# Kernel tuning notes

Measured on AMD Instinct MI355X. Metric: run time of the kernel, lower is better.

Reference implementation:

```python
import jax, jax.numpy as jnp
import numpy as np

ALPHA = 0.2          # LeakyReLU slope
NEG_BIG = -9e15      # mask value from the torch code
LN_EPS = 1e-5        # torch LayerNorm default eps
GAT_SCALE = 1.0


def _layer_norm(x, g, b):
    mu = x.mean(-1, keepdims=True)
    var = ((x - mu) ** 2).mean(-1, keepdims=True)
    return (x - mu) * jax.lax.rsqrt(var + LN_EPS) * g + b


def _gat_layer(h, adj, W, a, concat):
    # h: [B,N,Fin], adj: [N,N] weighted, W: [Fin,Fout], a: [2*Fout,1]
    Wh = jnp.einsum('bnf,fo->bno', h, W)                 # [B,N,Fout]
    Fo = W.shape[1]
    a_i, a_j = a[:Fo, 0], a[Fo:, 0]
    # e[b,i,j] = leakyrelu(Wh[b,i].a_i + Wh[b,j].a_j)  (== cat([Wh_i,Wh_j]) @ a)
    e = jax.nn.leaky_relu(
        (Wh @ a_i)[:, :, None] + (Wh @ a_j)[:, None, :], ALPHA)  # [B,N,N]
    att = jnp.where(adj[None, :, :] > 0, e, NEG_BIG)
    att = jax.nn.softmax(att, axis=2)
    att = att * adj[None, :, :]
    att = att / (att.sum(axis=2, keepdims=True) + 1e-8)
    h_prime = jnp.einsum('bij,bjo->bio', att, Wh)        # [B,N,Fout]
    return jax.nn.elu(h_prime) if concat else h_prime


def setup_inputs() -> dict:
    B, N, H, ID = 1024, 128, 64, 8
    GIN = 1 + ID  # node_feat_dim = 0
    key = jax.random.key(0)
    ks = jax.random.split(key, 20)
    # sparse weighted adjacency with self-loops
    w = jax.random.uniform(ks[0], (N, N))
    m = (jax.random.uniform(ks[1], (N, N)) < 0.3).astype(jnp.float32)
    adj = w * m + jnp.eye(N, dtype=jnp.float32)
    sc = lambda k, s: jax.random.normal(k, s, jnp.float32) * 0.1
    return {
        'c_values': jax.random.normal(ks[2], (B, N), jnp.float32),
        'adj': adj,
        'agent_emb': sc(ks[3], (N, ID)),
        'W1': sc(ks[4], (GIN, H)), 'a1': sc(ks[5], (2 * H, 1)),
        'W2': sc(ks[6], (H, H)),   'a2': sc(ks[7], (2 * H, 1)),
        'ln1_g': jnp.ones((H,)), 'ln1_b': jnp.zeros((H,)),
        'ln2_g': jnp.ones((H,)), 'ln2_b': jnp.zeros((H,)),
        'head_gat_w': sc(ks[8], (H, 1)), 'head_gat_b': jnp.zeros((1,)),
        'mlp1_w': sc(ks[9], (N, H)),  'mlp1_b': jnp.zeros((H,)),
        'mlp2_w': sc(ks[10], (H, H)), 'mlp2_b': jnp.zeros((H,)),
        'head_mlp_w': sc(ks[11], (H, 1)), 'head_mlp_b': jnp.zeros((1,)),
        'gate1_w': sc(ks[12], (N, H)), 'gate1_b': jnp.zeros((H,)),
        'gate2_w': sc(ks[13], (H, 1)), 'gate2_b': jnp.full((1,), -5.0),
    }


def reference(c_values, adj, agent_emb, W1, a1, W2, a2,
              ln1_g, ln1_b, ln2_g, ln2_b, head_gat_w, head_gat_b,
              mlp1_w, mlp1_b, mlp2_w, mlp2_b, head_mlp_w, head_mlp_b,
              gate1_w, gate1_b, gate2_w, gate2_b):
    B, N = c_values.shape
    # node features: [c_value, agent_id_embedding]
    id_feat = jnp.broadcast_to(agent_emb[None], (B, N, agent_emb.shape[1]))
    x_g = jnp.concatenate([c_values[..., None], id_feat], axis=-1)  # [B,N,9]
    h1 = _gat_layer(x_g, adj, W1, a1, concat=True)
    h1 = _layer_norm(h1, ln1_g, ln1_b)
    h2 = _gat_layer(h1, adj, W2, a2, concat=False)
    h = jax.nn.relu(h2 + h1)
    h = _layer_norm(h, ln2_g, ln2_b)
    q_gat = h.mean(axis=1) @ head_gat_w + head_gat_b                # [B,1]
    x_m = jax.nn.relu(c_values @ mlp1_w + mlp1_b)
    x_m = jax.nn.relu(x_m @ mlp2_w + mlp2_b)
    q_mlp = x_m @ head_mlp_w + head_mlp_b                           # [B,1]
    gate = jax.nn.sigmoid(
        jax.nn.relu(c_values @ gate1_w + gate1_b) @ gate2_w + gate2_b)
    return q_mlp + gate * GAT_SCALE * q_gat
```

## Files before the change

### kernel.cpp

```cpp
#include <hip/hip_runtime.h>

typedef unsigned short u16;
typedef unsigned int u32;
typedef short v8s __attribute__((ext_vector_type(8)));
typedef float v4f __attribute__((ext_vector_type(4)));

__device__ __forceinline__ float bflo(u32 d){union{u32 i;float f;}u;u.i=d<<16;return u.f;}
__device__ __forceinline__ float bfhi(u32 d){union{u32 i;float f;}u;u.i=d&0xffff0000u;return u.f;}
__device__ __forceinline__ u16 f2bfr(float f){union{float f;u32 i;}u;u.f=f;return (u16)((u.i+0x8000u)>>16);}
__device__ __forceinline__ u32 pk2bf(float a,float b){
    union{float f;u32 i;}ua,ub; ua.f=a; ub.f=b;
    return ((ua.i+0x8000u)>>16)|((ub.i+0x8000u)&0xffff0000u);
}
__device__ __forceinline__ v8s pack8(const float* w){
    union { uint4 u; v8s v; } c;
    c.u.x = pk2bf(w[0],w[1]); c.u.y = pk2bf(w[2],w[3]);
    c.u.z = pk2bf(w[4],w[5]); c.u.w = pk2bf(w[6],w[7]);
    return c.v;
}

__device__ __forceinline__ void flash_att(
    int wv, int l15, int q4,
    const float* __restrict__ ADJ,
    const float* __restrict__ sEi, const float* __restrict__ sFi,
    const float* __restrict__ sEj, const float* __restrict__ sFj,
    const u16* __restrict__ sWhT,
    v4f acc[2][4], float invD[2])
{
    const int r0 = 16*wv + l15, r1 = r0 + 64;
    const float Ei0 = sEi[r0], Fi0 = sFi[r0];
    const float Ei1 = sEi[r1], Fi1 = sFi[r1];
    float D0 = 0.f, D1 = 0.f;
    #pragma unroll
    for (int s = 0; s < 2; ++s)
        #pragma unroll
        for (int ct = 0; ct < 4; ++ct) acc[s][ct] = (v4f){0.f,0.f,0.f,0.f};

    for (int ks = 0; ks < 4; ++ks) {
        const int ko = ks*32 + q4*8;
        float w0[8], w1[8];
        #pragma unroll
        for (int half = 0; half < 2; ++half) {
            float4 E4 = *(const float4*)(sEj + ko + 4*half);
            float4 F4 = *(const float4*)(sFj + ko + 4*half);
            float4 a0 = *(const float4*)(ADJ + r0*128 + ko + 4*half);
            float4 a1 = *(const float4*)(ADJ + r1*128 + ko + 4*half);
            float Ev[4] = {E4.x,E4.y,E4.z,E4.w};
            float Fv[4] = {F4.x,F4.y,F4.z,F4.w};
            float av0[4] = {a0.x,a0.y,a0.z,a0.w};
            float av1[4] = {a1.x,a1.y,a1.z,a1.w};
            #pragma unroll
            for (int k = 0; k < 4; ++k) {
                float p0 = Ei0 * Ev[k], q0 = Fi0 * Fv[k];
                float s0 = (p0 >= 1.f) ? p0 : q0;
                float x0 = s0 * av0[k];
                float p1 = Ei1 * Ev[k], q1 = Fi1 * Fv[k];
                float s1 = (p1 >= 1.f) ? p1 : q1;
                float x1 = s1 * av1[k];
                w0[half*4 + k] = x0; w1[half*4 + k] = x1;
                D0 += x0; D1 += x1;
            }
        }
        v8s A0 = pack8(w0), A1 = pack8(w1);
        #pragma unroll
        for (int ct = 0; ct < 4; ++ct) {
            v8s B = *(const v8s*)(sWhT + (16*ct + l15)*136 + ko);
            acc[0][ct] = __builtin_amdgcn_mfma_f32_16x16x32_bf16(A0, B, acc[0][ct], 0,0,0);
            acc[1][ct] = __builtin_amdgcn_mfma_f32_16x16x32_bf16(A1, B, acc[1][ct], 0,0,0);
        }
    }
    D0 += __shfl_xor(D0, 16); D0 += __shfl_xor(D0, 32);
    D1 += __shfl_xor(D1, 16); D1 += __shfl_xor(D1, 32);
    invD[0] = 1.f / D0; invD[1] = 1.f / D1;
}

__global__ __launch_bounds__(256, 4) void graphmixer_kernel(
    const float* __restrict__ C,
    const float* __restrict__ ADJ,
    const float* __restrict__ EMB,
    const float* __restrict__ W1,
    const float* __restrict__ A1,
    const float* __restrict__ W2,
    const float* __restrict__ A2,
    const float* __restrict__ LN1G, const float* __restrict__ LN1B,
    const float* __restrict__ LN2G, const float* __restrict__ LN2B,
    const float* __restrict__ HGW,  const float* __restrict__ HGB,
    const float* __restrict__ MLP1W, const float* __restrict__ MLP1B,
    const float* __restrict__ MLP2W, const float* __restrict__ MLP2B,
    const float* __restrict__ HMW,  const float* __restrict__ HMB,
    const float* __restrict__ G1W,  const float* __restrict__ G1B,
    const float* __restrict__ G2W,  const float* __restrict__ G2B,
    float* __restrict__ OUT)
{
    const int b = blockIdx.x, t = threadIdx.x;
    const int lane = t & 63, wv = t >> 6;
    const int l15 = lane & 15, q4 = lane >> 4;

    __shared__ __align__(16) unsigned char smem[40096];
    u16*   sWhT = (u16*)(smem);
    u16*   sH1  = (u16*)(smem + 17408);
    float* sEi  = (float*)(smem + 35840);
    float* sFi  = (float*)(smem + 36352);
    float* sEj  = (float*)(smem + 36864);
    float* sFj  = (float*)(smem + 37376);
    float* colp = (float*)(smem + 37888);
    float* sScr = (float*)(smem + 38912);
    float* v2i  = (float*)(smem + 39456);
    float* v2j  = (float*)(smem + 39712);
    float* v1i  = (float*)(smem + 39968);
    float* v1j  = (float*)(smem + 40032);
    float* sEmb = (float*)(smem + 17408);
    float* sC   = (float*)(smem + 21504);

    const float* Cb = C + b*128;

    if (wv == 0) {
        #pragma unroll
        for (int q = 0; q < 4; ++q)
            ((float4*)sEmb)[lane + 64*q] = ((const float4*)EMB)[lane + 64*q];
        if (lane < 32) ((float4*)sC)[lane] = ((const float4*)Cb)[lane];
        if (lane >= 32 && lane < 41) {
            int f = lane - 32; float a = 0.f;
            for (int q = 0; q < 16; ++q) {
                float4 w = *(const float4*)(W1 + f*64 + q*4);
                float4 x = *(const float4*)(A1 + q*4);
                a += w.x*x.x + w.y*x.y + w.z*x.z + w.w*x.w;
            }
            v1i[f] = a;
        } else if (lane >= 48 && lane < 57) {
            int f = lane - 48; float a = 0.f;
            for (int q = 0; q < 16; ++q) {
                float4 w = *(const float4*)(W1 + f*64 + q*4);
                float4 x = *(const float4*)(A1 + 64 + q*4);
                a += w.x*x.x + w.y*x.y + w.z*x.z + w.w*x.w;
            }
            v1j[f] = a;
        }
    } else if (wv == 3) {
        float ai = 0.f, aj = 0.f;
        for (int q = 0; q < 16; ++q) {
            float4 w  = *(const float4*)(W2 + lane*64 + q*4);
            float4 xi = *(const float4*)(A2 + q*4);
            float4 xj = *(const float4*)(A2 + 64 + q*4);
            ai += w.x*xi.x + w.y*xi.y + w.z*xi.z + w.w*xi.w;
            aj += w.x*xj.x + w.y*xj.y + w.z*xj.z + w.w*xj.w;
        }
        v2i[lane] = ai; v2j[lane] = aj;
    } else if (wv == 1) {
        float a = 0.f;
        for (int k = 0; k < 128; k += 4) {
            float4 c4 = *(const float4*)(Cb + k);
            a += c4.x*MLP1W[k*64+lane] + c4.y*MLP1W[(k+1)*64+lane]
               + c4.z*MLP1W[(k+2)*64+lane] + c4.w*MLP1W[(k+3)*64+lane];
        }
        sScr[lane] = fmaxf(a + MLP1B[lane], 0.f);
        float a2 = 0.f;
        for (int k = 0; k < 64; ++k) a2 += sScr[k] * MLP2W[k*64 + lane];
        float x2 = fmaxf(a2 + MLP2B[lane], 0.f);
        float p1 = x2 * HMW[lane];
        #pragma unroll
        for (int off = 32; off >= 1; off >>= 1) p1 += __shfl_down(p1, off);
        if (lane == 0) sScr[128] = p1 + HMB[0];
    } else {
        float a = 0.f;
        for (int k = 0; k < 128; k += 4) {
            float4 c4 = *(const float4*)(Cb + k);
            a += c4.x*G1W[k*64+lane] + c4.y*G1W[(k+1)*64+lane]
               + c4.z*G1W[(k+2)*64+lane] + c4.w*G1W[(k+3)*64+lane];
        }
        float g1 = fmaxf(a + G1B[lane], 0.f);
        float p2 = g1 * G2W[lane];
        #pragma unroll
        for (int off = 32; off >= 1; off >>= 1) p2 += __shfl_down(p2, off);
        if (lane == 0) sScr[129] = 1.f / (1.f + __expf(-(p2 + G2B[0])));
    }
    __syncthreads();

    {
        const int o = lane, cc = wv;
        float w1f[9];
        #pragma unroll
        for (int f = 0; f < 9; ++f) w1f[f] = W1[f*64 + o];
        float whv[32];
        for (int i = 0; i < 32; ++i) {
            const int ig = cc*32 + i;
            float a = sC[ig] * w1f[0];
            float4 e0 = *(const float4*)(sEmb + ig*8);
            float4 e1 = *(const float4*)(sEmb + ig*8 + 4);
            a += e0.x*w1f[1] + e0.y*w1f[2] + e0.z*w1f[3] + e0.w*w1f[4];
            a += e1.x*w1f[5] + e1.y*w1f[6] + e1.z*w1f[7] + e1.w*w1f[8];
            whv[i] = a;
        }
        u32 p[16];
        #pragma unroll
        for (int q = 0; q < 16; ++q) p[q] = pk2bf(whv[2*q], whv[2*q+1]);
        uint4* dst = (uint4*)(sWhT + o*136 + cc*32);
        dst[0] = ((uint4*)p)[0]; dst[1] = ((uint4*)p)[1];
        dst[2] = ((uint4*)p)[2]; dst[3] = ((uint4*)p)[3];
    }
    if (t < 128) {
        float c = sC[t];
        float4 e0 = *(const float4*)(sEmb + t*8);
        float4 e1 = *(const float4*)(sEmb + t*8 + 4);
        float ei = c*v1i[0] + e0.x*v1i[1]+e0.y*v1i[2]+e0.z*v1i[3]+e0.w*v1i[4]
                            + e1.x*v1i[5]+e1.y*v1i[6]+e1.z*v1i[7]+e1.w*v1i[8];
        float ej = c*v1j[0] + e0.x*v1j[1]+e0.y*v1j[2]+e0.z*v1j[3]+e0.w*v1j[4]
                            + e1.x*v1j[5]+e1.y*v1j[6]+e1.z*v1j[7]+e1.w*v1j[8];
        sEi[t] = __expf(ei); sFi[t] = __expf(0.2f*ei);
        sEj[t] = __expf(ej); sFj[t] = __expf(0.2f*ej);
    }
    __syncthreads();

    {
        v4f acc[2][4]; float invD[2];
        flash_att(wv, l15, q4, ADJ, sEi, sFi, sEj, sFj, sWhT, acc, invD);

        float g4[4], b4[4];
        #pragma unroll
        for (int ct = 0; ct < 4; ++ct) { g4[ct] = LN1G[16*ct + l15]; b4[ct] = LN1B[16*ct + l15]; }
        #pragma unroll
        for (int s = 0; s < 2; ++s) {
            const int rbase = 16*(wv + 4*s) + 4*q4;
            #pragma unroll
            for (int reg = 0; reg < 4; ++reg) {
                const int row = rbase + reg;
                const float rd = __shfl(invD[s], 4*q4 + reg);
                float x[4], s1 = 0.f, s2 = 0.f;
                #pragma unroll
                for (int ct = 0; ct < 4; ++ct) {
                    float v = acc[s][ct][reg] * rd;
                    v = (v > 0.f) ? v : (__expf(v) - 1.f);
                    x[ct] = v; s1 += v; s2 += v*v;
                }
                s1 += __shfl_xor(s1, 1); s2 += __shfl_xor(s2, 1);
                s1 += __shfl_xor(s1, 2); s2 += __shfl_xor(s2, 2);
                s1 += __shfl_xor(s1, 4); s2 += __shfl_xor(s2, 4);
                s1 += __shfl_xor(s1, 8); s2 += __shfl_xor(s2, 8);
                const float mean = s1 * (1.f/64.f);
                const float var  = s2 * (1.f/64.f) - mean*mean;
                const float rstd = rsqrtf(var + 1e-5f);
                #pragma unroll
                for (int ct = 0; ct < 4; ++ct) {
                    float h = (x[ct] - mean) * rstd * g4[ct] + b4[ct];
                    sH1[row*72 + 16*ct + l15] = f2bfr(h);
                }
            }
        }
    }
    __syncthreads();

    if (t < 128) {
        float ei = 0.f, ej = 0.f;
        const u16* hrow = sH1 + t*72;
        for (int q = 0; q < 16; ++q) {
            uint2 d = *(const uint2*)(hrow + q*4);
            float h0 = bflo(d.x), h1v = bfhi(d.x), h2 = bflo(d.y), h3 = bfhi(d.y);
            ei += h0*v2i[q*4+0] + h1v*v2i[q*4+1] + h2*v2i[q*4+2] + h3*v2i[q*4+3];
            ej += h0*v2j[q*4+0] + h1v*v2j[q*4+1] + h2*v2j[q*4+2] + h3*v2j[q*4+3];
        }
        sEi[t] = __expf(ei); sFi[t] = __expf(0.2f*ei);
        sEj[t] = __expf(ej); sFj[t] = __expf(0.2f*ej);
    }
    {
        v4f acc2[2][4];
        #pragma unroll
        for (int s = 0; s < 2; ++s)
            #pragma unroll
            for (int ct = 0; ct < 4; ++ct) acc2[s][ct] = (v4f){0.f,0.f,0.f,0.f};
        #pragma unroll
        for (int ks = 0; ks < 2; ++ks) {
            const int kb = ks*32 + q4*8;
            v8s Bf[4];
            #pragma unroll
            for (int ct = 0; ct < 4; ++ct) {
                const float* wp = W2 + kb*64 + 16*ct + l15;
                float w8[8];
                #pragma unroll
                for (int j = 0; j < 8; ++j) w8[j] = wp[j*64];
                Bf[ct] = pack8(w8);
            }
            #pragma unroll
            for (int s = 0; s < 2; ++s) {
                v8s A = *(const v8s*)(sH1 + (16*(wv+4*s) + l15)*72 + kb);
                #pragma unroll
                for (int ct = 0; ct < 4; ++ct)
                    acc2[s][ct] = __builtin_amdgcn_mfma_f32_16x16x32_bf16(A, Bf[ct], acc2[s][ct], 0,0,0);
            }
        }
        #pragma unroll
        for (int s = 0; s < 2; ++s) {
            const int rb = 16*(wv+4*s) + 4*q4;
            #pragma unroll
            for (int ct = 0; ct < 4; ++ct) {
                const int col = 16*ct + l15;
                uint2 p;
                p.x = pk2bf(acc2[s][ct][0], acc2[s][ct][1]);
                p.y = pk2bf(acc2[s][ct][2], acc2[s][ct][3]);
                *(uint2*)(sWhT + col*136 + rb) = p;
            }
        }
    }
    __syncthreads();

    {
        v4f acc[2][4]; float invD[2];
        flash_att(wv, l15, q4, ADJ, sEi, sFi, sEj, sFj, sWhT, acc, invD);

        float g4[4], b4[4], colsum[4];
        #pragma unroll
        for (int ct = 0; ct < 4; ++ct) {
            g4[ct] = LN2G[16*ct + l15]; b4[ct] = LN2B[16*ct + l15]; colsum[ct] = 0.f;
        }
        #pragma unroll
        for (int s = 0; s < 2; ++s) {
            const int rbase = 16*(wv + 4*s) + 4*q4;
            #pragma unroll
            for (int reg = 0; reg < 4; ++reg) {
                const int row = rbase + reg;
                const float rd = __shfl(invD[s], 4*q4 + reg);
                float x[4], s1 = 0.f, s2 = 0.f;
                #pragma unroll
                for (int ct = 0; ct < 4; ++ct) {
                    float h1v = bflo((u32)sH1[row*72 + 16*ct + l15]);
                    float v = fmaxf(acc[s][ct][reg] * rd + h1v, 0.f);
                    x[ct] = v; s1 += v; s2 += v*v;
                }
                s1 += __shfl_xor(s1, 1); s2 += __shfl_xor(s2, 1);
                s1 += __shfl_xor(s1, 2); s2 += __shfl_xor(s2, 2);
                s1 += __shfl_xor(s1, 4); s2 += __shfl_xor(s2, 4);
                s1 += __shfl_xor(s1, 8); s2 += __shfl_xor(s2, 8);
                const float mean = s1 * (1.f/64.f);
                const float var  = s2 * (1.f/64.f) - mean*mean;
                const float rstd = rsqrtf(var + 1e-5f);
                #pragma unroll
                for (int ct = 0; ct < 4; ++ct)
                    colsum[ct] += (x[ct] - mean) * rstd * g4[ct] + b4[ct];
            }
        }
        #pragma unroll
        for (int ct = 0; ct < 4; ++ct) {
            colsum[ct] += __shfl_xor(colsum[ct], 16);
            colsum[ct] += __shfl_xor(colsum[ct], 32);
        }
        if (lane < 16) {
            #pragma unroll
            for (int ct = 0; ct < 4; ++ct) colp[wv*64 + ct*16 + lane] = colsum[ct];
        }
    }
    __syncthreads();

    if (wv == 0) {
        float s = colp[lane] + colp[64 + lane] + colp[128 + lane] + colp[192 + lane];
        float p = s * (1.f/128.f) * HGW[lane];
        #pragma unroll
        for (int off = 32; off >= 1; off >>= 1) p += __shfl_down(p, off);
        if (lane == 0) OUT[b] = sScr[128] + sScr[129] * (p + HGB[0]);
    }
}

extern "C" void kernel_launch(void* const* d_in, const int* in_sizes, int n_in,
                              void* d_out, int out_size, void* d_ws, size_t ws_size,
                              hipStream_t stream) {
    (void)n_in; (void)out_size; (void)d_ws; (void)ws_size;
    const float* C     = (const float*)d_in[0];
    const float* ADJ   = (const float*)d_in[1];
    const float* EMB   = (const float*)d_in[2];
    const float* W1    = (const float*)d_in[3];
    const float* A1    = (const float*)d_in[4];
    const float* W2    = (const float*)d_in[5];
    const float* A2    = (const float*)d_in[6];
    const float* LN1G  = (const float*)d_in[7];
    const float* LN1B  = (const float*)d_in[8];
    const float* LN2G  = (const float*)d_in[9];
    const float* LN2B  = (const float*)d_in[10];
    const float* HGW   = (const float*)d_in[11];
    const float* HGB   = (const float*)d_in[12];
    const float* MLP1W = (const float*)d_in[13];
    const float* MLP1B = (const float*)d_in[14];
    const float* MLP2W = (const float*)d_in[15];
    const float* MLP2B = (const float*)d_in[16];
    const float* HMW   = (const float*)d_in[17];
    const float* HMB   = (const float*)d_in[18];
    const float* G1W   = (const float*)d_in[19];
    const float* G1B   = (const float*)d_in[20];
    const float* G2W   = (const float*)d_in[21];
    const float* G2B   = (const float*)d_in[22];

    const int B = in_sizes[0] / 128;

    graphmixer_kernel<<<dim3(B), dim3(256), 0, stream>>>(
        C, ADJ, EMB, W1, A1, W2, A2, LN1G, LN1B, LN2G, LN2B,
        HGW, HGB, MLP1W, MLP1B, MLP2W, MLP2B, HMW, HMB,
        G1W, G1B, G2W, G2B, (float*)d_out);
}
```

Measured before the change: 131.4 us.

## Compute attention row sums via MFMA, use hardware bf16 packing, keep h1 in registers

Computes the attention denominators with an extra MFMA against a ones vector instead of scalar adds and cross-lane shuffles, which also places the sums in the same layout as the output accumulators. The LeakyReLU branch is replaced with an fmaxf, and the manual bf16 rounding is swapped for the HIP packed conversion intrinsic. The LayerNorm-1 output is kept packed in registers so the residual add in layer 2 does not re-read shared memory. Several small dot-product loops get multiple accumulators to break dependency chains. Risks include higher register pressure from the extra accumulators and h1 cache, plus slight numerical differences because the denominator is now summed from bf16-rounded weights.

```diff
diff --git a/kernel.cpp b/kernel.cpp
--- a/kernel.cpp
+++ b/kernel.cpp
@@ -1,4 +1,5 @@
 #include <hip/hip_runtime.h>
+#include <hip/hip_bf16.h>
 
 typedef unsigned short u16;
 typedef unsigned int u32;
@@ -7,15 +8,14 @@
 
 __device__ __forceinline__ float bflo(u32 d){union{u32 i;float f;}u;u.i=d<<16;return u.f;}
 __device__ __forceinline__ float bfhi(u32 d){union{u32 i;float f;}u;u.i=d&0xffff0000u;return u.f;}
-__device__ __forceinline__ u16 f2bfr(float f){union{float f;u32 i;}u;u.f=f;return (u16)((u.i+0x8000u)>>16);}
-__device__ __forceinline__ u32 pk2bf(float a,float b){
-    union{float f;u32 i;}ua,ub; ua.f=a; ub.f=b;
-    return ((ua.i+0x8000u)>>16)|((ub.i+0x8000u)&0xffff0000u);
+__device__ __forceinline__ u32 cvtpk(float a, float b){
+    __hip_bfloat162 h = __float22bfloat162_rn(make_float2(a, b));
+    u32 r; __builtin_memcpy(&r, &h, sizeof(r)); return r;
 }
 __device__ __forceinline__ v8s pack8(const float* w){
     union { uint4 u; v8s v; } c;
-    c.u.x = pk2bf(w[0],w[1]); c.u.y = pk2bf(w[2],w[3]);
-    c.u.z = pk2bf(w[4],w[5]); c.u.w = pk2bf(w[6],w[7]);
+    c.u.x = cvtpk(w[0],w[1]); c.u.y = cvtpk(w[2],w[3]);
+    c.u.z = cvtpk(w[4],w[5]); c.u.w = cvtpk(w[6],w[7]);
     return c.v;
 }
 
@@ -25,16 +25,18 @@
     const float* __restrict__ sEi, const float* __restrict__ sFi,
     const float* __restrict__ sEj, const float* __restrict__ sFj,
     const u16* __restrict__ sWhT,
-    v4f acc[2][4], float invD[2])
+    v4f acc[2][4], v4f accD[2])
 {
     const int r0 = 16*wv + l15, r1 = r0 + 64;
     const float Ei0 = sEi[r0], Fi0 = sFi[r0];
     const float Ei1 = sEi[r1], Fi1 = sFi[r1];
-    float D0 = 0.f, D1 = 0.f;
+    const v8s ONES = {16256,16256,16256,16256,16256,16256,16256,16256};
     #pragma unroll
-    for (int s = 0; s < 2; ++s)
+    for (int s = 0; s < 2; ++s) {
+        accD[s] = (v4f){0.f,0.f,0.f,0.f};
         #pragma unroll
         for (int ct = 0; ct < 4; ++ct) acc[s][ct] = (v4f){0.f,0.f,0.f,0.f};
+    }
 
     for (int ks = 0; ks < 4; ++ks) {
         const int ko = ks*32 + q4*8;
@@ -51,17 +53,13 @@
             float av1[4] = {a1.x,a1.y,a1.z,a1.w};
             #pragma unroll
             for (int k = 0; k < 4; ++k) {
-                float p0 = Ei0 * Ev[k], q0 = Fi0 * Fv[k];
-                float s0 = (p0 >= 1.f) ? p0 : q0;
-                float x0 = s0 * av0[k];
-                float p1 = Ei1 * Ev[k], q1 = Fi1 * Fv[k];
-                float s1 = (p1 >= 1.f) ? p1 : q1;
-                float x1 = s1 * av1[k];
-                w0[half*4 + k] = x0; w1[half*4 + k] = x1;
-                D0 += x0; D1 += x1;
+                w0[half*4 + k] = fmaxf(Ei0*Ev[k], Fi0*Fv[k]) * av0[k];
+                w1[half*4 + k] = fmaxf(Ei1*Ev[k], Fi1*Fv[k]) * av1[k];
             }
         }
         v8s A0 = pack8(w0), A1 = pack8(w1);
+        accD[0] = __builtin_amdgcn_mfma_f32_16x16x32_bf16(A0, ONES, accD[0], 0,0,0);
+        accD[1] = __builtin_amdgcn_mfma_f32_16x16x32_bf16(A1, ONES, accD[1], 0,0,0);
         #pragma unroll
         for (int ct = 0; ct < 4; ++ct) {
             v8s B = *(const v8s*)(sWhT + (16*ct + l15)*136 + ko);
@@ -69,9 +67,6 @@
             acc[1][ct] = __builtin_amdgcn_mfma_f32_16x16x32_bf16(A1, B, acc[1][ct], 0,0,0);
         }
     }
-    D0 += __shfl_xor(D0, 16); D0 += __shfl_xor(D0, 32);
-    D1 += __shfl_xor(D1, 16); D1 += __shfl_xor(D1, 32);
-    invD[0] = 1.f / D0; invD[1] = 1.f / D1;
 }
 
 __global__ __launch_bounds__(256, 4) void graphmixer_kernel(
@@ -120,55 +115,70 @@
             ((float4*)sEmb)[lane + 64*q] = ((const float4*)EMB)[lane + 64*q];
         if (lane < 32) ((float4*)sC)[lane] = ((const float4*)Cb)[lane];
         if (lane >= 32 && lane < 41) {
-            int f = lane - 32; float a = 0.f;
-            for (int q = 0; q < 16; ++q) {
+            int f = lane - 32; float a0 = 0.f, a1 = 0.f;
+            for (int q = 0; q < 16; q += 2) {
                 float4 w = *(const float4*)(W1 + f*64 + q*4);
                 float4 x = *(const float4*)(A1 + q*4);
-                a += w.x*x.x + w.y*x.y + w.z*x.z + w.w*x.w;
-            }
-            v1i[f] = a;
+                a0 += w.x*x.x + w.y*x.y + w.z*x.z + w.w*x.w;
+                float4 w2 = *(const float4*)(W1 + f*64 + (q+1)*4);
+                float4 x2 = *(const float4*)(A1 + (q+1)*4);
+                a1 += w2.x*x2.x + w2.y*x2.y + w2.z*x2.z + w2.w*x2.w;
+            }
+            v1i[f] = a0 + a1;
         } else if (lane >= 48 && lane < 57) {
-            int f = lane - 48; float a = 0.f;
-            for (int q = 0; q < 16; ++q) {
+            int f = lane - 48; float a0 = 0.f, a1 = 0.f;
+            for (int q = 0; q < 16; q += 2) {
                 float4 w = *(const float4*)(W1 + f*64 + q*4);
                 float4 x = *(const float4*)(A1 + 64 + q*4);
-                a += w.x*x.x + w.y*x.y + w.z*x.z + w.w*x.w;
-            }
-            v1j[f] = a;
+                a0 += w.x*x.x + w.y*x.y + w.z*x.z + w.w*x.w;
+                float4 w2 = *(const float4*)(W1 + f*64 + (q+1)*4);
+                float4 x2 = *(const float4*)(A1 + 64 + (q+1)*4);
+                a1 += w2.x*x2.x + w2.y*x2.y + w2.z*x2.z + w2.w*x2.w;
+            }
+            v1j[f] = a0 + a1;
         }
     } else if (wv == 3) {
-        float ai = 0.f, aj = 0.f;
+        float ai0 = 0.f, ai1 = 0.f, aj0 = 0.f, aj1 = 0.f;
         for (int q = 0; q < 16; ++q) {
             float4 w  = *(const float4*)(W2 + lane*64 + q*4);
             float4 xi = *(const float4*)(A2 + q*4);
             float4 xj = *(const float4*)(A2 + 64 + q*4);
-            ai += w.x*xi.x + w.y*xi.y + w.z*xi.z + w.w*xi.w;
-            aj += w.x*xj.x + w.y*xj.y + w.z*xj.z + w.w*xj.w;
-        }
-        v2i[lane] = ai; v2j[lane] = aj;
+            ai0 += w.x*xi.x + w.y*xi.y; ai1 += w.z*xi.z + w.w*xi.w;
+            aj0 += w.x*xj.x + w.y*xj.y; aj1 += w.z*xj.z + w.w*xj.w;
+        }
+        v2i[lane] = ai0 + ai1; v2j[lane] = aj0 + aj1;
     } else if (wv == 1) {
-        float a = 0.f;
+        float a0 = 0.f, a1 = 0.f, a2v = 0.f, a3 = 0.f;
         for (int k = 0; k < 128; k += 4) {
             float4 c4 = *(const float4*)(Cb + k);
-            a += c4.x*MLP1W[k*64+lane] + c4.y*MLP1W[(k+1)*64+lane]
-               + c4.z*MLP1W[(k+2)*64+lane] + c4.w*MLP1W[(k+3)*64+lane];
-        }
-        sScr[lane] = fmaxf(a + MLP1B[lane], 0.f);
-        float a2 = 0.f;
-        for (int k = 0; k < 64; ++k) a2 += sScr[k] * MLP2W[k*64 + lane];
-        float x2 = fmaxf(a2 + MLP2B[lane], 0.f);
+            a0  += c4.x*MLP1W[k*64+lane];
+            a1  += c4.y*MLP1W[(k+1)*64+lane];
+            a2v += c4.z*MLP1W[(k+2)*64+lane];
+            a3  += c4.w*MLP1W[(k+3)*64+lane];
+        }
+        sScr[lane] = fmaxf(a0+a1+a2v+a3 + MLP1B[lane], 0.f);
+        float b0 = 0.f, b1 = 0.f, b2 = 0.f, b3 = 0.f;
+        for (int k = 0; k < 64; k += 4) {
+            b0 += sScr[k]  *MLP2W[k*64 + lane];
+            b1 += sScr[k+1]*MLP2W[(k+1)*64 + lane];
+            b2 += sScr[k+2]*MLP2W[(k+2)*64 + lane];
+            b3 += sScr[k+3]*MLP2W[(k+3)*64 + lane];
+        }
+        float x2 = fmaxf(b0+b1+b2+b3 + MLP2B[lane], 0.f);
         float p1 = x2 * HMW[lane];
         #pragma unroll
         for (int off = 32; off >= 1; off >>= 1) p1 += __shfl_down(p1, off);
         if (lane == 0) sScr[128] = p1 + HMB[0];
     } else {
-        float a = 0.f;
+        float a0 = 0.f, a1 = 0.f, a2v = 0.f, a3 = 0.f;
         for (int k = 0; k < 128; k += 4) {
             float4 c4 = *(const float4*)(Cb + k);
-            a += c4.x*G1W[k*64+lane] + c4.y*G1W[(k+1)*64+lane]
-               + c4.z*G1W[(k+2)*64+lane] + c4.w*G1W[(k+3)*64+lane];
-        }
-        float g1 = fmaxf(a + G1B[lane], 0.f);
+            a0  += c4.x*G1W[k*64+lane];
+            a1  += c4.y*G1W[(k+1)*64+lane];
+            a2v += c4.z*G1W[(k+2)*64+lane];
+            a3  += c4.w*G1W[(k+3)*64+lane];
+        }
+        float g1 = fmaxf(a0+a1+a2v+a3 + G1B[lane], 0.f);
         float p2 = g1 * G2W[lane];
         #pragma unroll
         for (int off = 32; off >= 1; off >>= 1) p2 += __shfl_down(p2, off);
@@ -193,7 +203,7 @@
         }
         u32 p[16];
         #pragma unroll
-        for (int q = 0; q < 16; ++q) p[q] = pk2bf(whv[2*q], whv[2*q+1]);
+        for (int q = 0; q < 16; ++q) p[q] = cvtpk(whv[2*q], whv[2*q+1]);
         uint4* dst = (uint4*)(sWhT + o*136 + cc*32);
         dst[0] = ((uint4*)p)[0]; dst[1] = ((uint4*)p)[1];
         dst[2] = ((uint4*)p)[2]; dst[3] = ((uint4*)p)[3];
@@ -211,9 +221,11 @@
     }
     __syncthreads();
 
+    u32 h1p[2][4][2];
+
     {
-        v4f acc[2][4]; float invD[2];
-        flash_att(wv, l15, q4, ADJ, sEi, sFi, sEj, sFj, sWhT, acc, invD);
+        v4f acc[2][4]; v4f accD[2];
+        flash_att(wv, l15, q4, ADJ, sEi, sFi, sEj, sFj, sWhT, acc, accD);
 
         float g4[4], b4[4];
         #pragma unroll
@@ -224,7 +236,7 @@
             #pragma unroll
             for (int reg = 0; reg < 4; ++reg) {
                 const int row = rbase + reg;
-                const float rd = __shfl(invD[s], 4*q4 + reg);
+                const float rd = 1.f / accD[s][reg];
                 float x[4], s1 = 0.f, s2 = 0.f;
                 #pragma unroll
                 for (int ct = 0; ct < 4; ++ct) {
@@ -239,11 +251,17 @@
                 const float mean = s1 * (1.f/64.f);
                 const float var  = s2 * (1.f/64.f) - mean*mean;
                 const float rstd = rsqrtf(var + 1e-5f);
-                #pragma unroll
-                for (int ct = 0; ct < 4; ++ct) {
-                    float h = (x[ct] - mean) * rstd * g4[ct] + b4[ct];
-                    sH1[row*72 + 16*ct + l15] = f2bfr(h);
-                }
+                float h[4];
+                #pragma unroll
+                for (int ct = 0; ct < 4; ++ct)
+                    h[ct] = (x[ct] - mean) * rstd * g4[ct] + b4[ct];
+                const u32 p01 = cvtpk(h[0], h[1]);
+                const u32 p23 = cvtpk(h[2], h[3]);
+                h1p[s][reg][0] = p01; h1p[s][reg][1] = p23;
+                sH1[row*72 +      l15] = (u16)(p01 & 0xffffu);
+                sH1[row*72 + 16 + l15] = (u16)(p01 >> 16);
+                sH1[row*72 + 32 + l15] = (u16)(p23 & 0xffffu);
+                sH1[row*72 + 48 + l15] = (u16)(p23 >> 16);
             }
         }
     }
@@ -294,8 +312,8 @@
             for (int ct = 0; ct < 4; ++ct) {
                 const int col = 16*ct + l15;
                 uint2 p;
-                p.x = pk2bf(acc2[s][ct][0], acc2[s][ct][1]);
-                p.y = pk2bf(acc2[s][ct][2], acc2[s][ct][3]);
+                p.x = cvtpk(acc2[s][ct][0], acc2[s][ct][1]);
+                p.y = cvtpk(acc2[s][ct][2], acc2[s][ct][3]);
                 *(uint2*)(sWhT + col*136 + rb) = p;
             }
         }
@@ -303,8 +321,8 @@
     __syncthreads();
 
     {
-        v4f acc[2][4]; float invD[2];
-        flash_att(wv, l15, q4, ADJ, sEi, sFi, sEj, sFj, sWhT, acc, invD);
+        v4f acc[2][4]; v4f accD[2];
+        flash_att(wv, l15, q4, ADJ, sEi, sFi, sEj, sFj, sWhT, acc, accD);
 
         float g4[4], b4[4], colsum[4];
         #pragma unroll
@@ -313,15 +331,14 @@
         }
         #pragma unroll
         for (int s = 0; s < 2; ++s) {
-            const int rbase = 16*(wv + 4*s) + 4*q4;
             #pragma unroll
             for (int reg = 0; reg < 4; ++reg) {
-                const int row = rbase + reg;
-                const float rd = __shfl(invD[s], 4*q4 + reg);
+                const float rd = 1.f / accD[s][reg];
                 float x[4], s1 = 0.f, s2 = 0.f;
                 #pragma unroll
                 for (int ct = 0; ct < 4; ++ct) {
-                    float h1v = bflo((u32)sH1[row*72 + 16*ct + l15]);
+                    const u32 pw = h1p[s][reg][ct >> 1];
+                    const float h1v = (ct & 1) ? bfhi(pw) : bflo(pw);
                     float v = fmaxf(acc[s][ct][reg] * rd + h1v, 0.f);
                     x[ct] = v; s1 += v; s2 += v*v;
                 }
```

Measured after the change: 131.1 us. Within noise of the previous version (-0.3%).
